# Kernel tuning notes

Measured on AMD Instinct MI355X. Metric: run time of the kernel, lower is better.

Reference implementation:

```python
import jax, jax.numpy as jnp
import numpy as np

B, C, H, W = 8, 512, 32, 32
HEADS = 8
DIM = C // HEADS
EPS = 1e-5


def setup_inputs() -> dict:
    key = jax.random.key(0)
    ks = jax.random.split(key, 7)
    scale = 1.0 / np.sqrt(C)
    return {
        "x": jax.random.normal(ks[0], (B, C, H, W), dtype=jnp.float32),
        "gn_gamma": jnp.ones((C,), dtype=jnp.float32),
        "gn_beta": jnp.zeros((C,), dtype=jnp.float32),
        "w_qkv": jax.random.normal(ks[1], (3 * HEADS * DIM, C), dtype=jnp.float32) * scale,
        "b_qkv": jax.random.normal(ks[2], (3 * HEADS * DIM,), dtype=jnp.float32) * 0.01,
        "w_proj": jax.random.normal(ks[3], (C, HEADS * DIM), dtype=jnp.float32) * scale,
        "b_proj": jax.random.normal(ks[4], (C,), dtype=jnp.float32) * 0.01,
    }


def reference(x, gn_gamma, gn_beta, w_qkv, b_qkv, w_proj, b_proj):
    b, c, h, w = x.shape
    n = h * w
    # GroupNorm with 1 group: normalize over (C,H,W) per sample (biased var)
    mu = jnp.mean(x, axis=(1, 2, 3), keepdims=True)
    var = jnp.var(x, axis=(1, 2, 3), keepdims=True)
    xn = (x - mu) * jax.lax.rsqrt(var + EPS)
    xn = xn * gn_gamma[None, :, None, None] + gn_beta[None, :, None, None]
    # 1x1 conv QKV projection == channel matmul
    qkv = jnp.einsum('bchw,oc->bohw', xn, w_qkv) + b_qkv[None, :, None, None]
    qkv = qkv.reshape(b, 3, HEADS, DIM, n)  # matches view(B,3*heads,dim,N).chunk(3,dim=1)
    q, k, v = qkv[:, 0], qkv[:, 1], qkv[:, 2]  # each (B, heads, dim, N)
    # scale uses full channel count C, as in the source (C ** -0.5)
    dot = jnp.einsum('bhdn,bhdm->bhnm', q, k) * (c ** -0.5)
    attn = jax.nn.softmax(dot, axis=-1)
    vals = jnp.einsum('bhnm,bhdm->bhdn', attn, v)  # (B, heads, dim, N)
    vals = vals.reshape(b, HEADS * DIM, h, w)
    return jnp.einsum('bchw,oc->bohw', vals, w_proj) + b_proj[None, :, None, None]
```

## Files before the change

### kernel.cpp

```cpp
#include <hip/hip_runtime.h>
#include <hip/hip_bf16.h>
#include <math.h>

#define NB 8
#define NC 512
#define NN 1024
#define NHEADS 8
#define EPSV 1e-5f
#define SC2F 0.06376351307f

typedef __attribute__((ext_vector_type(8))) short bf16x8;
typedef __attribute__((ext_vector_type(4))) short bf16x4;
typedef __attribute__((ext_vector_type(4))) float f32x4;
typedef __attribute__((ext_vector_type(16))) float f32x16;

#define MFMA16(a,b,c) __builtin_amdgcn_mfma_f32_16x16x32_bf16(a,b,c,0,0,0)
#define MFMA32(a,b,c) __builtin_amdgcn_mfma_f32_32x32x16_bf16(a,b,c,0,0,0)

static __device__ __forceinline__ short f2bf(float f) {
    __hip_bfloat16 h = __float2bfloat16(f);
    return *reinterpret_cast<short*>(&h);
}

static __device__ __forceinline__ unsigned cvt_pk_bf16(float lo, float hi) {
    unsigned r;
    asm("v_cvt_pk_bf16_f32 %0, %1, %2" : "=v"(r) : "v"(lo), "v"(hi));
    return r;
}

static __device__ __forceinline__ void gload16(const void* g, void* l) {
    __builtin_amdgcn_global_load_lds((const __attribute__((address_space(1))) void*)g,
                                     (__attribute__((address_space(3))) void*)l, 16, 0, 0);
}

#define WS_PART_SUM 0
#define WS_PART_SQ  1024
#define WS_XNT   4096
#define WS_QT    (WS_XNT  + 2097152)
#define WS_KT    (WS_QT   + 2097152)
#define WS_V     (WS_KT   + 2097152)
#define WS_VALST (WS_V    + 2097152)
#define WS_WQB   (WS_VALST+ 2097152)
#define WS_WPB   (WS_WQB  + 393216)

__global__ __launch_bounds__(256) void prep_kernel(const float* __restrict__ x,
                                                   const float* __restrict__ wq,
                                                   const float* __restrict__ wp,
                                                   float* __restrict__ ws) {
    int blk = blockIdx.x;
    int b = blk >> 6;
    int s = blk & 63;
    const float* xb = x + (size_t)b * (NC * NN) + (size_t)s * 8192;
    float sum = 0.f, sq = 0.f;
    for (int i = threadIdx.x; i < 2048; i += 256) {
        float4 v = ((const float4*)xb)[i];
        sum += v.x + v.y + v.z + v.w;
        sq  += v.x*v.x + v.y*v.y + v.z*v.z + v.w*v.w;
    }
    #pragma unroll
    for (int off = 32; off; off >>= 1) {
        sum += __shfl_down(sum, off);
        sq  += __shfl_down(sq,  off);
    }
    __shared__ float s1[4], s2[4];
    int wave = threadIdx.x >> 6, lane = threadIdx.x & 63;
    if (lane == 0) { s1[wave] = sum; s2[wave] = sq; }

    #pragma unroll
    for (int r = 0; r < 2; r++) {
        int i = blk * 512 + threadIdx.x * 2 + r;
        const float* src;
        __hip_bfloat16* d;
        if (i < 196608) { src = wq; d = (__hip_bfloat16*)(ws + WS_WQB); }
        else            { src = wp; d = (__hip_bfloat16*)(ws + WS_WPB); i -= 196608; }
        float4 v = ((const float4*)src)[i];
        bf16x4 w;
        w[0] = f2bf(v.x); w[1] = f2bf(v.y); w[2] = f2bf(v.z); w[3] = f2bf(v.w);
        *(bf16x4*)(d + (size_t)i*4) = w;
    }

    __syncthreads();
    if (threadIdx.x == 0) {
        float a = 0.f, c2 = 0.f;
        #pragma unroll
        for (int w = 0; w < 4; w++) { a += s1[w]; c2 += s2[w]; }
        ws[WS_PART_SUM + b*64 + s] = a;
        ws[WS_PART_SQ  + b*64 + s] = c2;
    }
}

__global__ __launch_bounds__(256) void normalize_t(const float* __restrict__ x,
                                                   const float* __restrict__ gamma,
                                                   const float* __restrict__ beta,
                                                   const float* __restrict__ ws,
                                                   __hip_bfloat16* __restrict__ xnT) {
    int nt = blockIdx.x & 15, ct = (blockIdx.x >> 4) & 7, b = blockIdx.x >> 7;
    __shared__ __hip_bfloat16 tb[64][72];
    float s = 0.f, q = 0.f;
    const float4* ps = (const float4*)(ws + WS_PART_SUM + b*64);
    const float4* pq = (const float4*)(ws + WS_PART_SQ  + b*64);
    #pragma unroll
    for (int i = 0; i < 16; i++) {
        float4 a = ps[i]; s += a.x + a.y + a.z + a.w;
        float4 c = pq[i]; q += c.x + c.y + c.z + c.w;
    }
    const float inv = 1.f / (float)(NC * NN);
    float mu   = s * inv;
    float var  = q * inv - mu * mu;
    float rstd = rsqrtf(var + EPSV);

    const float* xb = x + ((size_t)b*512 + ct*64)*1024 + nt*64;
    int t = threadIdx.x;
    int cl = t >> 4, n4 = (t & 15) * 4;
    #pragma unroll
    for (int i = 0; i < 4; i++) {
        int c = i*16 + cl;
        float gm = gamma[ct*64 + c];
        float g = gm * rstd;
        float be = beta[ct*64 + c] - mu * g;
        float4 v = *(const float4*)(xb + (size_t)c*1024 + n4);
        tb[n4+0][c] = __float2bfloat16(v.x*g + be);
        tb[n4+1][c] = __float2bfloat16(v.y*g + be);
        tb[n4+2][c] = __float2bfloat16(v.z*g + be);
        tb[n4+3][c] = __float2bfloat16(v.w*g + be);
    }
    __syncthreads();
    #pragma unroll
    for (int i = 0; i < 2; i++) {
        int idx = i*256 + t;
        int n = idx >> 3, c8 = (idx & 7) * 8;
        *(bf16x8*)(xnT + ((size_t)b*1024 + nt*64 + n)*512 + ct*64 + c8) =
            *(const bf16x8*)&tb[n][c8];
    }
}

__global__ __launch_bounds__(256) void gemm_qkv(const __hip_bfloat16* __restrict__ Aw,
                                                const __hip_bfloat16* __restrict__ Bx,
                                                const float* __restrict__ bias,
                                                __hip_bfloat16* __restrict__ QTx,
                                                __hip_bfloat16* __restrict__ KTx,
                                                __hip_bfloat16* __restrict__ Vx) {
    __shared__ __align__(16) __hip_bfloat16 lds_raw[12288];
    const int bx = blockIdx.x;
    const int swz = (bx & 7) * 192 + (bx >> 3);
    const int nt = swz & 15;
    const int ot = (swz >> 4) % 12;
    const int bb = swz / 192;
    const int o0 = ot * 128, n0 = nt * 64;

    const int t = threadIdx.x, wv = t >> 6, l = t & 63;
    const int lr = l & 31, lh = l >> 5;

    const __hip_bfloat16* Ag = Aw + (size_t)o0 * 512;
    const __hip_bfloat16* Bg = Bx + ((size_t)bb * 1024 + n0) * 512;
    __hip_bfloat16* Ab = lds_raw;
    __hip_bfloat16* Bb = lds_raw + 128*64;

    f32x16 acc[2];
    #pragma unroll
    for (int ni = 0; ni < 2; ni++)
        #pragma unroll
        for (int r = 0; r < 16; r++) acc[ni][r] = 0.f;

    for (int k0 = 0; k0 < 512; k0 += 64) {
        __syncthreads();
        #pragma unroll
        for (int p = 0; p < 4; p++) {
            int idx = t + p*256;
            int row = idx >> 3, sl = idx & 7;
            int sk = sl ^ (row & 7);
            gload16(Ag + (size_t)row*512 + k0 + sk*8, Ab + idx*8);
        }
        #pragma unroll
        for (int p = 0; p < 2; p++) {
            int idx = t + p*256;
            int row = idx >> 3, sl = idx & 7;
            int sk = sl ^ (row & 7);
            gload16(Bg + (size_t)row*512 + k0 + sk*8, Bb + idx*8);
        }
        __syncthreads();
        #pragma unroll
        for (int ks = 0; ks < 4; ks++) {
            int arow = wv*32 + lr;
            bf16x8 af = *(const bf16x8*)(Ab + arow*64 + (((ks*2 + lh) ^ (arow & 7)) * 8));
            #pragma unroll
            for (int ni = 0; ni < 2; ni++) {
                int brow = ni*32 + lr;
                bf16x8 bfr = *(const bf16x8*)(Bb + brow*64 + (((ks*2 + lh) ^ (brow & 7)) * 8));
                acc[ni] = MFMA32(af, bfr, acc[ni]);
            }
        }
    }

    int sec = o0 >> 9;
    if (sec == 2) {
        int od0 = o0 & 511;
        int mperm = ((lr & 12) << 1) + ((lr & 16) >> 2) + (lr & 3);
        #pragma unroll
        for (int q = 0; q < 4; q++) {
            int ob = wv*32 + 8*q + 4*lh;
            float4 bv = *(const float4*)(bias + o0 + ob);
            #pragma unroll
            for (int j = 0; j < 4; j++) {
                int ol = od0 + ob + j;
                int h = ol >> 6, d = ol & 63;
                __hip_bfloat16* dst = Vx + ((size_t)((bb<<3) + h)*64 + d)*1024;
                #pragma unroll
                for (int ni = 0; ni < 2; ni++) {
                    int nn = n0 + ni*32 + mperm;
                    dst[nn] = __float2bfloat16(acc[ni][q*4+j] + bv[j]);
                }
            }
        }
    } else {
        const float qs = (sec == 0) ? SC2F : 1.0f;
        __syncthreads();
        __hip_bfloat16* tb = lds_raw;
        #pragma unroll
        for (int q = 0; q < 4; q++) {
            int ob = wv*32 + 8*q + 4*lh;
            float4 bv = *(const float4*)(bias + o0 + ob);
            #pragma unroll
            for (int ni = 0; ni < 2; ni++) {
                int nn = ni*32 + lr;
                bf16x4 w;
                #pragma unroll
                for (int j = 0; j < 4; j++) w[j] = f2bf((acc[ni][q*4+j] + bv[j]) * qs);
                *(bf16x4*)&tb[(size_t)nn*136 + ob] = w;
            }
        }
        __syncthreads();
        __hip_bfloat16* dst0 = (sec == 0) ? QTx : KTx;
        int h0 = (o0 & 511) >> 6;
        #pragma unroll
        for (int i = 0; i < 4; i++) {
            int idx = i*256 + t;
            int n = idx >> 4, rem = idx & 15;
            int hh = rem >> 3, slot = rem & 7;
            int hf32 = (slot & 4) << 3;
            int g4   = (slot & 3) << 2;
            bf16x4 lo = *(const bf16x4*)&tb[(size_t)n*136 + hh*64 + hf32 + g4];
            bf16x4 hi = *(const bf16x4*)&tb[(size_t)n*136 + hh*64 + hf32 + 16 + g4];
            bf16x8 w;
            w[0]=lo[0]; w[1]=lo[1]; w[2]=lo[2]; w[3]=lo[3];
            w[4]=hi[0]; w[5]=hi[1]; w[6]=hi[2]; w[7]=hi[3];
            *(bf16x8*)(dst0 + ((size_t)((bb<<3) + h0 + hh)*1024 + n0 + n)*64 + slot*8) = w;
        }
    }
}

__global__ __launch_bounds__(256) void gemm_proj(const __hip_bfloat16* __restrict__ Aw,
                                                 const __hip_bfloat16* __restrict__ Bx,
                                                 const float* __restrict__ bias,
                                                 float* __restrict__ Yout) {
    __shared__ __align__(16) __hip_bfloat16 lds_raw[12288];
    const int bx = blockIdx.x;
    const int swz = (bx & 7) * 64 + (bx >> 3);
    const int nt = swz & 15;
    const int ot = (swz >> 4) & 3;
    const int bb = swz >> 6;
    const int o0 = ot * 128, n0 = nt * 64;

    const int t = threadIdx.x, wv = t >> 6, l = t & 63;
    const int lr = l & 31, lh = l >> 5;

    const __hip_bfloat16* Ag = Aw + (size_t)o0 * 512;
    const __hip_bfloat16* Bg = Bx + ((size_t)bb * 1024 + n0) * 512;
    __hip_bfloat16* Ab = lds_raw;
    __hip_bfloat16* Bb = lds_raw + 128*64;

    f32x16 acc[2];
    #pragma unroll
    for (int ni = 0; ni < 2; ni++)
        #pragma unroll
        for (int r = 0; r < 16; r++) acc[ni][r] = 0.f;

    for (int k0 = 0; k0 < 512; k0 += 64) {
        __syncthreads();
        #pragma unroll
        for (int p = 0; p < 4; p++) {
            int idx = t + p*256;
            int row = idx >> 3, sl = idx & 7;
            int sk = sl ^ (row & 7);
            gload16(Ag + (size_t)row*512 + k0 + sk*8, Ab + idx*8);
        }
        #pragma unroll
        for (int p = 0; p < 2; p++) {
            int idx = t + p*256;
            int row = idx >> 3, sl = idx & 7;
            int sk = sl ^ (row & 7);
            gload16(Bg + (size_t)row*512 + k0 + sk*8, Bb + idx*8);
        }
        __syncthreads();
        #pragma unroll
        for (int ks = 0; ks < 4; ks++) {
            int arow = wv*32 + lr;
            bf16x8 af = *(const bf16x8*)(Ab + arow*64 + (((ks*2 + lh) ^ (arow & 7)) * 8));
            #pragma unroll
            for (int ni = 0; ni < 2; ni++) {
                int brow = ni*32 + lr;
                bf16x8 bfr = *(const bf16x8*)(Bb + brow*64 + (((ks*2 + lh) ^ (brow & 7)) * 8));
                acc[ni] = MFMA32(af, bfr, acc[ni]);
            }
        }
    }

    #pragma unroll
    for (int q = 0; q < 4; q++) {
        int obase = o0 + wv*32 + 8*q + 4*lh;
        float4 bv = *(const float4*)(bias + obase);
        #pragma unroll
        for (int ni = 0; ni < 2; ni++) {
            int nn = n0 + ni*32 + lr;
            #pragma unroll
            for (int j = 0; j < 4; j++)
                Yout[((size_t)bb*512 + obase + j)*1024 + nn] = acc[ni][q*4+j] + bv[j];
        }
    }
}

__global__ __launch_bounds__(512) void attn_mfma(const __hip_bfloat16* __restrict__ QT,
                                                 const __hip_bfloat16* __restrict__ KT,
                                                 const __hip_bfloat16* __restrict__ Vb,
                                                 __hip_bfloat16* __restrict__ valsT) {
    const int bh = ((blockIdx.x & 7) << 3) | ((blockIdx.x >> 3) & 7);
    const int qt = blockIdx.x >> 6;
    const int t = threadIdx.x;
    const int wv = t >> 6, lane = t & 63;
    const int g = lane >> 4, li = lane & 15;

    const __hip_bfloat16* QTg = QT + (size_t)bh * NN * 64;
    const __hip_bfloat16* KTg = KT + (size_t)bh * NN * 64;
    const __hip_bfloat16* Vg  = Vb + (size_t)bh * 64 * NN;

    __shared__ __align__(16) __hip_bfloat16 k_ls[2*4096];
    __shared__ __align__(16) __hip_bfloat16 v_ls[2*4096];

    const int nq0 = qt*128 + wv*16;

    bf16x8 qf[2];
    {
        const __hip_bfloat16* qp = QTg + (size_t)(nq0 + li) * 64;
        qf[0] = *(const bf16x8*)(qp + 8*g);
        qf[1] = *(const bf16x8*)(qp + 32 + 8*g);
    }

    bf16x8 onesf;
    #pragma unroll
    for (int j = 0; j < 8; j++) onesf[j] = (short)0x3F80;

    float m_run = 0.0f;
    f32x4 o_acc[4], o_l;
    #pragma unroll
    for (int dt = 0; dt < 4; dt++) { o_acc[dt][0]=0.f; o_acc[dt][1]=0.f; o_acc[dt][2]=0.f; o_acc[dt][3]=0.f; }
    o_l[0]=0.f; o_l[1]=0.f; o_l[2]=0.f; o_l[3]=0.f;

    auto STAGE = [&](int buf, int ck) {
        const int mc0 = ck * 64;
        int row = t >> 3, sl = t & 7;
        int sk = sl ^ (row & 7);
        gload16(KTg + (size_t)(mc0+row)*64 + sk*8, k_ls + buf*4096 + t*8);
        gload16(Vg + (size_t)row*NN + mc0 + sk*8, v_ls + buf*4096 + t*8);
    };

    STAGE(0, 0);
    __syncthreads();
    int cur = 0;

    for (int ck = 0; ck < 16; ck++) {
        if (ck < 15) STAGE(cur ^ 1, ck + 1);

        const __hip_bfloat16* kb = k_ls + cur*4096;
        const __hip_bfloat16* vb = v_ls + cur*4096;

        f32x4 cini;
        cini[0] = -m_run; cini[1] = -m_run; cini[2] = -m_run; cini[3] = -m_run;
        f32x4 s_acc[4];
        __builtin_amdgcn_s_setprio(1);
        #pragma unroll
        for (int mt = 0; mt < 4; mt++) {
            f32x4 c = cini;
            #pragma unroll
            for (int hf = 0; hf < 2; hf++) {
                int row = mt*16 + li;
                int sl = ((hf<<2) + g) ^ (li & 7);
                bf16x8 kf = *(const bf16x8*)(kb + row*64 + sl*8);
                c = MFMA16(kf, qf[hf], c);
            }
            s_acc[mt] = c;
        }
        __builtin_amdgcn_s_setprio(0);

        float cmax = fmaxf(s_acc[0][0], s_acc[0][1]);
        cmax = fmaxf(fmaxf(cmax, s_acc[0][2]), s_acc[0][3]);
        cmax = fmaxf(fmaxf(cmax, s_acc[1][0]), s_acc[1][1]);
        cmax = fmaxf(fmaxf(cmax, s_acc[1][2]), s_acc[1][3]);
        cmax = fmaxf(fmaxf(cmax, s_acc[2][0]), s_acc[2][1]);
        cmax = fmaxf(fmaxf(cmax, s_acc[2][2]), s_acc[2][3]);
        cmax = fmaxf(fmaxf(cmax, s_acc[3][0]), s_acc[3][1]);
        cmax = fmaxf(fmaxf(cmax, s_acc[3][2]), s_acc[3][3]);
        cmax = fmaxf(cmax, __shfl_xor(cmax, 16));
        cmax = fmaxf(cmax, __shfl_xor(cmax, 32));

        if (ck == 0) {
            #pragma unroll
            for (int mt = 0; mt < 4; mt++) {
                s_acc[mt][0] -= cmax; s_acc[mt][1] -= cmax;
                s_acc[mt][2] -= cmax; s_acc[mt][3] -= cmax;
            }
            m_run = cmax;
        } else if (!__all(cmax <= 8.0f)) {
            float d = fmaxf(cmax, 0.0f);
            float resc = __builtin_amdgcn_exp2f(-d);
            f32x4 rv;
            #pragma unroll
            for (int r = 0; r < 4; r++) rv[r] = __shfl(resc, 4*g + r);
            #pragma unroll
            for (int dt = 0; dt < 4; dt++) {
                o_acc[dt][0]*=rv[0]; o_acc[dt][1]*=rv[1]; o_acc[dt][2]*=rv[2]; o_acc[dt][3]*=rv[3];
            }
            o_l[0]*=rv[0]; o_l[1]*=rv[1]; o_l[2]*=rv[2]; o_l[3]*=rv[3];
            #pragma unroll
            for (int mt = 0; mt < 4; mt++) {
                s_acc[mt][0] -= d; s_acc[mt][1] -= d;
                s_acc[mt][2] -= d; s_acc[mt][3] -= d;
            }
            m_run += d;
        }

        bf16x8 pf[2];
        #pragma unroll
        for (int ks = 0; ks < 2; ks++) {
            union { bf16x8 v; unsigned u[4]; } pk;
            #pragma unroll
            for (int d4 = 0; d4 < 4; d4++) {
                const int i0 = 8*ks + 2*d4, i1 = i0 + 1;
                float e0 = __builtin_amdgcn_exp2f(s_acc[i0>>2][i0&3]);
                float e1 = __builtin_amdgcn_exp2f(s_acc[i1>>2][i1&3]);
                pk.u[d4] = cvt_pk_bf16(e0, e1);
            }
            pf[ks] = pk.v;
        }

        __builtin_amdgcn_s_setprio(1);
        #pragma unroll
        for (int dt = 0; dt < 4; dt++) {
            #pragma unroll
            for (int ks = 0; ks < 2; ks++) {
                int row = dt*16 + li;
                int sl = ((ks<<2) + g) ^ (li & 7);
                bf16x8 vf = *(const bf16x8*)(vb + row*64 + sl*8);
                o_acc[dt] = MFMA16(pf[ks], vf, o_acc[dt]);
            }
        }
        o_l = MFMA16(pf[0], onesf, o_l);
        o_l = MFMA16(pf[1], onesf, o_l);
        __builtin_amdgcn_s_setprio(0);

        __syncthreads();
        cur ^= 1;
    }

    f32x4 lv;
    #pragma unroll
    for (int r = 0; r < 4; r++) lv[r] = 1.0f / o_l[r];
    const int bI = bh >> 3, hI = bh & 7;
    __hip_bfloat16* vt = valsT + (size_t)bI*1024*512 + hI*64;
    #pragma unroll
    for (int dt = 0; dt < 4; dt++)
        #pragma unroll
        for (int r = 0; r < 4; r++)
            vt[(size_t)(nq0 + 4*g + r)*512 + dt*16 + li] = __float2bfloat16(o_acc[dt][r]*lv[r]);
}

extern "C" void kernel_launch(void* const* d_in, const int* in_sizes, int n_in,
                              void* d_out, int out_size, void* d_ws, size_t ws_size,
                              hipStream_t stream) {
    const float* x      = (const float*)d_in[0];
    const float* gamma  = (const float*)d_in[1];
    const float* beta   = (const float*)d_in[2];
    const float* w_qkv  = (const float*)d_in[3];
    const float* b_qkv  = (const float*)d_in[4];
    const float* w_proj = (const float*)d_in[5];
    const float* b_proj = (const float*)d_in[6];
    float* ws   = (float*)d_ws;
    float* out  = (float*)d_out;
    __hip_bfloat16* xnT   = (__hip_bfloat16*)(ws + WS_XNT);
    __hip_bfloat16* QT    = (__hip_bfloat16*)(ws + WS_QT);
    __hip_bfloat16* KT    = (__hip_bfloat16*)(ws + WS_KT);
    __hip_bfloat16* Vx    = (__hip_bfloat16*)(ws + WS_V);
    __hip_bfloat16* valsT = (__hip_bfloat16*)(ws + WS_VALST);
    __hip_bfloat16* wqb   = (__hip_bfloat16*)(ws + WS_WQB);
    __hip_bfloat16* wpb   = (__hip_bfloat16*)(ws + WS_WPB);

    prep_kernel<<<dim3(512), dim3(256), 0, stream>>>(x, w_qkv, w_proj, ws);
    normalize_t<<<dim3(1024), dim3(256), 0, stream>>>(x, gamma, beta, ws, xnT);
    gemm_qkv<<<dim3(1536), dim3(256), 0, stream>>>(wqb, xnT, b_qkv, QT, KT, Vx);
    attn_mfma<<<dim3(512), dim3(512), 0, stream>>>(QT, KT, Vx, valsT);
    gemm_proj<<<dim3(512), dim3(256), 0, stream>>>(wpb, valsT, b_proj, out);
}
```

Before: 69.82 us.

## Fold GroupNorm into QKV GEMM epilogue and merge prep kernels

The separate stats and normalize kernels are merged into one prep kernel. It transposes raw x to bf16 and writes partial sums, while also folding gamma into the QKV weights and precomputing per-row sums of W*gamma and W*beta. The QKV GEMM then applies the normalization algebraically in its epilogue as rstd*acc + bias + sb - mu*rstd*sg. This removes one kernel launch and a full extra read of x. The trade-off is that the GEMM now multiplies unnormalized bf16 x, which can lose precision when the mean is large compared with the spread.

Result: faster. 68.31 us (median of 2 runs) (-2.2%).

```diff
diff --git a/kernel.cpp b/kernel.cpp
--- a/kernel.cpp
+++ b/kernel.cpp
@@ -35,112 +35,115 @@
 
 #define WS_PART_SUM 0
 #define WS_PART_SQ  1024
-#define WS_XNT   4096
-#define WS_QT    (WS_XNT  + 2097152)
+#define WS_SG       2048
+#define WS_SB       3584
+#define WS_XT    8192
+#define WS_QT    (WS_XT   + 2097152)
 #define WS_KT    (WS_QT   + 2097152)
 #define WS_V     (WS_KT   + 2097152)
 #define WS_VALST (WS_V    + 2097152)
 #define WS_WQB   (WS_VALST+ 2097152)
 #define WS_WPB   (WS_WQB  + 393216)
 
-__global__ __launch_bounds__(256) void prep_kernel(const float* __restrict__ x,
-                                                   const float* __restrict__ wq,
-                                                   const float* __restrict__ wp,
-                                                   float* __restrict__ ws) {
-    int blk = blockIdx.x;
-    int b = blk >> 6;
-    int s = blk & 63;
-    const float* xb = x + (size_t)b * (NC * NN) + (size_t)s * 8192;
-    float sum = 0.f, sq = 0.f;
-    for (int i = threadIdx.x; i < 2048; i += 256) {
-        float4 v = ((const float4*)xb)[i];
-        sum += v.x + v.y + v.z + v.w;
-        sq  += v.x*v.x + v.y*v.y + v.z*v.z + v.w*v.w;
-    }
-    #pragma unroll
-    for (int off = 32; off; off >>= 1) {
-        sum += __shfl_down(sum, off);
-        sq  += __shfl_down(sq,  off);
-    }
-    __shared__ float s1[4], s2[4];
-    int wave = threadIdx.x >> 6, lane = threadIdx.x & 63;
-    if (lane == 0) { s1[wave] = sum; s2[wave] = sq; }
-
-    #pragma unroll
-    for (int r = 0; r < 2; r++) {
-        int i = blk * 512 + threadIdx.x * 2 + r;
-        const float* src;
-        __hip_bfloat16* d;
-        if (i < 196608) { src = wq; d = (__hip_bfloat16*)(ws + WS_WQB); }
-        else            { src = wp; d = (__hip_bfloat16*)(ws + WS_WPB); i -= 196608; }
-        float4 v = ((const float4*)src)[i];
-        bf16x4 w;
-        w[0] = f2bf(v.x); w[1] = f2bf(v.y); w[2] = f2bf(v.z); w[3] = f2bf(v.w);
-        *(bf16x4*)(d + (size_t)i*4) = w;
-    }
-
-    __syncthreads();
-    if (threadIdx.x == 0) {
-        float a = 0.f, c2 = 0.f;
-        #pragma unroll
-        for (int w = 0; w < 4; w++) { a += s1[w]; c2 += s2[w]; }
-        ws[WS_PART_SUM + b*64 + s] = a;
-        ws[WS_PART_SQ  + b*64 + s] = c2;
-    }
-}
-
-__global__ __launch_bounds__(256) void normalize_t(const float* __restrict__ x,
-                                                   const float* __restrict__ gamma,
-                                                   const float* __restrict__ beta,
-                                                   const float* __restrict__ ws,
-                                                   __hip_bfloat16* __restrict__ xnT) {
-    int nt = blockIdx.x & 15, ct = (blockIdx.x >> 4) & 7, b = blockIdx.x >> 7;
-    __shared__ __hip_bfloat16 tb[64][72];
-    float s = 0.f, q = 0.f;
-    const float4* ps = (const float4*)(ws + WS_PART_SUM + b*64);
-    const float4* pq = (const float4*)(ws + WS_PART_SQ  + b*64);
-    #pragma unroll
-    for (int i = 0; i < 16; i++) {
-        float4 a = ps[i]; s += a.x + a.y + a.z + a.w;
-        float4 c = pq[i]; q += c.x + c.y + c.z + c.w;
-    }
-    const float inv = 1.f / (float)(NC * NN);
-    float mu   = s * inv;
-    float var  = q * inv - mu * mu;
-    float rstd = rsqrtf(var + EPSV);
-
-    const float* xb = x + ((size_t)b*512 + ct*64)*1024 + nt*64;
-    int t = threadIdx.x;
-    int cl = t >> 4, n4 = (t & 15) * 4;
-    #pragma unroll
-    for (int i = 0; i < 4; i++) {
-        int c = i*16 + cl;
-        float gm = gamma[ct*64 + c];
-        float g = gm * rstd;
-        float be = beta[ct*64 + c] - mu * g;
-        float4 v = *(const float4*)(xb + (size_t)c*1024 + n4);
-        tb[n4+0][c] = __float2bfloat16(v.x*g + be);
-        tb[n4+1][c] = __float2bfloat16(v.y*g + be);
-        tb[n4+2][c] = __float2bfloat16(v.z*g + be);
-        tb[n4+3][c] = __float2bfloat16(v.w*g + be);
-    }
-    __syncthreads();
-    #pragma unroll
-    for (int i = 0; i < 2; i++) {
-        int idx = i*256 + t;
-        int n = idx >> 3, c8 = (idx & 7) * 8;
-        *(bf16x8*)(xnT + ((size_t)b*1024 + nt*64 + n)*512 + ct*64 + c8) =
-            *(const bf16x8*)&tb[n][c8];
+__global__ __launch_bounds__(256) void prep2_kernel(const float* __restrict__ x,
+                                                    const float* __restrict__ gamma,
+                                                    const float* __restrict__ beta,
+                                                    const float* __restrict__ wq,
+                                                    const float* __restrict__ wp,
+                                                    float* __restrict__ ws,
+                                                    __hip_bfloat16* __restrict__ xT) {
+    const int blk = blockIdx.x;
+    const int t = threadIdx.x;
+    if (blk < 1024) {
+        int nt = blk & 15, ct = (blk >> 4) & 7, b = blk >> 7;
+        __shared__ __hip_bfloat16 tb[64][72];
+        __shared__ float s1[4], s2[4];
+        const float* xb = x + ((size_t)b*512 + ct*64)*1024 + nt*64;
+        int cl = t >> 4, n4 = (t & 15) * 4;
+        float sum = 0.f, sq = 0.f;
+        #pragma unroll
+        for (int i = 0; i < 4; i++) {
+            int c = i*16 + cl;
+            float4 v = *(const float4*)(xb + (size_t)c*1024 + n4);
+            sum += v.x + v.y + v.z + v.w;
+            sq  += v.x*v.x + v.y*v.y + v.z*v.z + v.w*v.w;
+            tb[n4+0][c] = __float2bfloat16(v.x);
+            tb[n4+1][c] = __float2bfloat16(v.y);
+            tb[n4+2][c] = __float2bfloat16(v.z);
+            tb[n4+3][c] = __float2bfloat16(v.w);
+        }
+        #pragma unroll
+        for (int off = 32; off; off >>= 1) {
+            sum += __shfl_down(sum, off);
+            sq  += __shfl_down(sq,  off);
+        }
+        int wave = t >> 6, lane = t & 63;
+        if (lane == 0) { s1[wave] = sum; s2[wave] = sq; }
+        __syncthreads();
+        #pragma unroll
+        for (int i = 0; i < 2; i++) {
+            int idx = i*256 + t;
+            int n = idx >> 3, c8 = (idx & 7) * 8;
+            *(bf16x8*)(xT + ((size_t)b*1024 + nt*64 + n)*512 + ct*64 + c8) =
+                *(const bf16x8*)&tb[n][c8];
+        }
+        if (t == 0) {
+            float a = 0.f, c2 = 0.f;
+            #pragma unroll
+            for (int w = 0; w < 4; w++) { a += s1[w]; c2 += s2[w]; }
+            ws[WS_PART_SUM + b*128 + (blk & 127)] = a;
+            ws[WS_PART_SQ  + b*128 + (blk & 127)] = c2;
+        }
+    } else {
+        const int wblk = blk - 1024;
+        __shared__ float sred[2][4];
+        __hip_bfloat16* wgb = (__hip_bfloat16*)(ws + WS_WQB);
+        const int wave = t >> 6, lane = t & 63;
+        float2 gm = *(const float2*)(gamma + 2*t);
+        float2 bt = *(const float2*)(beta + 2*t);
+        #pragma unroll
+        for (int rr = 0; rr < 3; rr++) {
+            int r = wblk*3 + rr;
+            float2 w = *(const float2*)(wq + (size_t)r*512 + 2*t);
+            float wg0 = w.x * gm.x, wg1 = w.y * gm.y;
+            *(unsigned*)(wgb + (size_t)r*512 + 2*t) = cvt_pk_bf16(wg0, wg1);
+            float sg = wg0 + wg1;
+            float sb = w.x*bt.x + w.y*bt.y;
+            #pragma unroll
+            for (int off = 32; off; off >>= 1) {
+                sg += __shfl_down(sg, off);
+                sb += __shfl_down(sb, off);
+            }
+            if (lane == 0) { sred[0][wave] = sg; sred[1][wave] = sb; }
+            __syncthreads();
+            if (t == 0) {
+                float tg = 0.f, tbv = 0.f;
+                #pragma unroll
+                for (int w2 = 0; w2 < 4; w2++) { tg += sred[0][w2]; tbv += sred[1][w2]; }
+                ws[WS_SG + r] = tg;
+                ws[WS_SB + r] = tbv;
+            }
+            __syncthreads();
+        }
+        if (t < 128) {
+            int i = wblk*128 + t;
+            float4 v = ((const float4*)wp)[i];
+            bf16x4 w4;
+            w4[0] = f2bf(v.x); w4[1] = f2bf(v.y); w4[2] = f2bf(v.z); w4[3] = f2bf(v.w);
+            *(bf16x4*)((__hip_bfloat16*)(ws + WS_WPB) + (size_t)i*4) = w4;
+        }
     }
 }
 
 __global__ __launch_bounds__(256) void gemm_qkv(const __hip_bfloat16* __restrict__ Aw,
                                                 const __hip_bfloat16* __restrict__ Bx,
                                                 const float* __restrict__ bias,
+                                                const float* __restrict__ ws,
                                                 __hip_bfloat16* __restrict__ QTx,
                                                 __hip_bfloat16* __restrict__ KTx,
                                                 __hip_bfloat16* __restrict__ Vx) {
     __shared__ __align__(16) __hip_bfloat16 lds_raw[12288];
+    __shared__ float stats_s[2];
     const int bx = blockIdx.x;
     const int swz = (bx & 7) * 192 + (bx >> 3);
     const int nt = swz & 15;
@@ -192,6 +195,28 @@
         }
     }
 
+    if (t < 64) {
+        const float* ps = ws + WS_PART_SUM + bb*128;
+        const float* pq = ws + WS_PART_SQ  + bb*128;
+        float s = ps[t] + ps[t + 64];
+        float q = pq[t] + pq[t + 64];
+        #pragma unroll
+        for (int off = 32; off; off >>= 1) {
+            s += __shfl_down(s, off);
+            q += __shfl_down(q, off);
+        }
+        if (t == 0) {
+            const float inv = 1.f / (float)(NC * NN);
+            float mu  = s * inv;
+            float var = q * inv - mu * mu;
+            stats_s[0] = mu;
+            stats_s[1] = rsqrtf(var + EPSV);
+        }
+    }
+    __syncthreads();
+    const float mu = stats_s[0], rstd = stats_s[1];
+    const float murs = mu * rstd;
+
     int sec = o0 >> 9;
     if (sec == 2) {
         int od0 = o0 & 511;
@@ -199,16 +224,19 @@
         #pragma unroll
         for (int q = 0; q < 4; q++) {
             int ob = wv*32 + 8*q + 4*lh;
-            float4 bv = *(const float4*)(bias + o0 + ob);
+            float4 bv  = *(const float4*)(bias + o0 + ob);
+            float4 sb4 = *(const float4*)(ws + WS_SB + o0 + ob);
+            float4 sg4 = *(const float4*)(ws + WS_SG + o0 + ob);
             #pragma unroll
             for (int j = 0; j < 4; j++) {
+                float bcor = bv[j] + sb4[j] - murs * sg4[j];
                 int ol = od0 + ob + j;
                 int h = ol >> 6, d = ol & 63;
                 __hip_bfloat16* dst = Vx + ((size_t)((bb<<3) + h)*64 + d)*1024;
                 #pragma unroll
                 for (int ni = 0; ni < 2; ni++) {
                     int nn = n0 + ni*32 + mperm;
-                    dst[nn] = __float2bfloat16(acc[ni][q*4+j] + bv[j]);
+                    dst[nn] = __float2bfloat16(rstd * acc[ni][q*4+j] + bcor);
                 }
             }
         }
@@ -219,13 +247,18 @@
         #pragma unroll
         for (int q = 0; q < 4; q++) {
             int ob = wv*32 + 8*q + 4*lh;
-            float4 bv = *(const float4*)(bias + o0 + ob);
+            float4 bv  = *(const float4*)(bias + o0 + ob);
+            float4 sb4 = *(const float4*)(ws + WS_SB + o0 + ob);
+            float4 sg4 = *(const float4*)(ws + WS_SG + o0 + ob);
             #pragma unroll
             for (int ni = 0; ni < 2; ni++) {
                 int nn = ni*32 + lr;
                 bf16x4 w;
                 #pragma unroll
-                for (int j = 0; j < 4; j++) w[j] = f2bf((acc[ni][q*4+j] + bv[j]) * qs);
+                for (int j = 0; j < 4; j++) {
+                    float bcor = bv[j] + sb4[j] - murs * sg4[j];
+                    w[j] = f2bf((rstd * acc[ni][q*4+j] + bcor) * qs);
+                }
                 *(bf16x4*)&tb[(size_t)nn*136 + ob] = w;
             }
         }
@@ -485,7 +518,7 @@
     const float* b_proj = (const float*)d_in[6];
     float* ws   = (float*)d_ws;
     float* out  = (float*)d_out;
-    __hip_bfloat16* xnT   = (__hip_bfloat16*)(ws + WS_XNT);
+    __hip_bfloat16* xT    = (__hip_bfloat16*)(ws + WS_XT);
     __hip_bfloat16* QT    = (__hip_bfloat16*)(ws + WS_QT);
     __hip_bfloat16* KT    = (__hip_bfloat16*)(ws + WS_KT);
     __hip_bfloat16* Vx    = (__hip_bfloat16*)(ws + WS_V);
@@ -493,9 +526,8 @@
     __hip_bfloat16* wqb   = (__hip_bfloat16*)(ws + WS_WQB);
     __hip_bfloat16* wpb   = (__hip_bfloat16*)(ws + WS_WPB);
 
-    prep_kernel<<<dim3(512), dim3(256), 0, stream>>>(x, w_qkv, w_proj, ws);
-    normalize_t<<<dim3(1024), dim3(256), 0, stream>>>(x, gamma, beta, ws, xnT);
-    gemm_qkv<<<dim3(1536), dim3(256), 0, stream>>>(wqb, xnT, b_qkv, QT, KT, Vx);
+    prep2_kernel<<<dim3(1536), dim3(256), 0, stream>>>(x, gamma, beta, w_qkv, w_proj, ws, xT);
+    gemm_qkv<<<dim3(1536), dim3(256), 0, stream>>>(wqb, xT, b_qkv, ws, QT, KT, Vx);
     attn_mfma<<<dim3(512), dim3(512), 0, stream>>>(QT, KT, Vx, valsT);
     gemm_proj<<<dim3(512), dim3(256), 0, stream>>>(wpb, valsT, b_proj, out);
 }
```
